# Performance work log

Measured on AMD Instinct MI355X. Metric: run time of the kernel, lower is better.

The kernel has to match this reference:

```python
import jax, jax.numpy as jnp
import numpy as np

D_MODEL = 1024
D_INNER = 2048   # expand=2
D_STATE = 16
D_CONV = 4
DT_RANK = 64     # ceil(d_model/16)
B_SZ = 2
L_SEQ = 2048
EPS = 1e-6


def setup_inputs() -> dict:
    key = jax.random.key(0)
    ks = jax.random.split(key, 9)
    def g(k, shape, scale=0.02):
        return jax.random.normal(k, shape, jnp.float32) * scale
    return {
        "x": jax.random.normal(ks[0], (B_SZ, L_SEQ, D_MODEL), jnp.float32),
        "ln_gamma": jnp.ones((D_MODEL,), jnp.float32),
        "ln_beta": jnp.zeros((D_MODEL,), jnp.float32),
        "in_proj_w": g(ks[1], (2 * D_INNER, D_MODEL)),
        "conv_w": g(ks[2], (D_INNER, 1, D_CONV), 0.1),
        "conv_b": g(ks[3], (D_INNER,), 0.1),
        "x_proj_w": g(ks[4], (DT_RANK + 2 * D_STATE, D_INNER)),
        "dt_proj_w": g(ks[5], (D_INNER, DT_RANK), 0.1),
        "dt_proj_b": g(ks[6], (D_INNER,), 0.1),
        "A_log": jnp.log(jnp.broadcast_to(jnp.arange(1, D_STATE + 1, dtype=jnp.float32), (D_INNER, D_STATE))),
        "D": jnp.ones((D_INNER,), jnp.float32),
        "out_proj_w": g(ks[7], (D_MODEL, D_INNER)),
    }


def _silu(v):
    return v * jax.nn.sigmoid(v)


def reference(x, ln_gamma, ln_beta, in_proj_w, conv_w, conv_b, x_proj_w,
              dt_proj_w, dt_proj_b, A_log, D, out_proj_w):
    B, L, _ = x.shape
    # LayerNorm (eps=1e-6)
    mu = x.mean(-1, keepdims=True)
    var = x.var(-1, keepdims=True)
    h = (x - mu) / jnp.sqrt(var + EPS) * ln_gamma + ln_beta
    # in_proj -> (B, 2*d_inner, L)
    xz = jnp.einsum('bld,ed->bel', h, in_proj_w)
    u, z = jnp.split(xz, 2, axis=1)
    # depthwise causal conv1d (padding=d_conv-1, then [..., :L]) + SiLU
    up = jnp.pad(u, ((0, 0), (0, 0), (D_CONV - 1, 0)))
    uc = jax.lax.conv_general_dilated(
        up, conv_w, (1,), 'VALID',
        dimension_numbers=('NCH', 'OIH', 'NCH'),
        feature_group_count=D_INNER)
    uc = _silu(uc + conv_b[None, :, None])  # (B, d_inner, L)
    # x_proj -> dt, B, C
    x_dbl = jnp.einsum('bdl,ed->ble', uc, x_proj_w)
    dt, Bm, Cm = jnp.split(x_dbl, [DT_RANK, DT_RANK + D_STATE], axis=-1)
    delta = jnp.einsum('blr,dr->bdl', dt, dt_proj_w) + dt_proj_b[None, :, None]
    delta = jax.nn.softplus(delta)  # delta_softplus=True with dt_proj bias
    A = -jnp.exp(A_log)  # (d_inner, d_state)
    deltaA = jnp.exp(jnp.einsum('bdl,dn->bdln', delta, A))
    Bm = jnp.transpose(Bm, (0, 2, 1))  # (B, n, L)
    Cm = jnp.transpose(Cm, (0, 2, 1))  # (B, n, L)
    deltaB_u = jnp.einsum('bdl,bnl,bdl->bdln', delta, Bm, uc)

    def step(state, inp):
        dA, dBu, Ct = inp  # (B,d,n), (B,d,n), (B,n)
        state = dA * state + dBu
        y = jnp.einsum('bdn,bn->bd', state, Ct)
        return state, y

    init = jnp.zeros((B, D_INNER, D_STATE), jnp.float32)
    _, ys = jax.lax.scan(
        step, init,
        (jnp.moveaxis(deltaA, 2, 0), jnp.moveaxis(deltaB_u, 2, 0), jnp.moveaxis(Cm, 2, 0)))
    y = jnp.moveaxis(ys, 0, 2)  # (B, d_inner, L)
    y = y + uc * D[None, :, None]
    y = y * _silu(z)
    out = jnp.einsum('bdl,ed->ble', y, out_proj_w)
    return out + x  # residual
```

## Files before the change

### kernel.cpp

```cpp
#include <hip/hip_runtime.h>
#include <hip/hip_bf16.h>

#define D_MODEL 1024
#define D_INNER 2048
#define D_STATE 16
#define D_CONV  4
#define DT_RANK 64
#define B_SZ    2
#define L_SEQ   2048
#define NTOK    (B_SZ * L_SEQ)
#define XD      (DT_RANK + 2 * D_STATE)
#define NCHUNK  64
#define TC      (L_SEQ / NCHUNK)
#define SPLITK  8

#define WS_U     0
#define WS_Z     16777216
#define WS_UC    33554432
#define WS_DY    50331648
#define WS_XDBL  67108864
#define WS_FLAG  67895296
#define WS_NEED  67895552
#define WS_W     67895552
#define OFF_INW  0
#define OFF_OUTW 8388608
#define OFF_XW   12582912
#define OFF_DTW  12976128
#define WS_FULL  81133824

typedef __attribute__((ext_vector_type(8))) short short8;
typedef __attribute__((ext_vector_type(4))) float float4v;

#define GAS __attribute__((address_space(1)))
#define LAS __attribute__((address_space(3)))
__device__ __forceinline__ void gload_lds16(const ushort* g, ushort* l) {
    __builtin_amdgcn_global_load_lds((const GAS uint*)g, (LAS uint*)l, 16, 0, 0);
}

__device__ __forceinline__ float bf2f_u(ushort u) {
    union { uint i; float f; } c; c.i = ((uint)u) << 16; return c.f;
}
__device__ __forceinline__ float u2f(uint u) {
    union { uint i; float f; } c; c.i = u; return c.f;
}
__device__ __forceinline__ ushort f2bf_u(float f) {
    union { float f; uint i; } c; c.f = f;
    uint r = c.i + 0x7FFFu + ((c.i >> 16) & 1u);
    return (ushort)(r >> 16);
}
__device__ __forceinline__ float silu_f(float v) {
    return v * __builtin_amdgcn_rcpf(1.f + __expf(-v));
}
__device__ __forceinline__ float softplus_f(float v) {
    return (v > 15.f) ? v : __logf(1.f + __expf(v));
}
__device__ __forceinline__ int sniff_bf16(const ushort* __restrict__ x) {
    int cnt = 0;
    #pragma unroll
    for (int i = 0; i < 128; i += 2) {
        int e = (x[i] >> 7) & 0xFF;
        cnt += (e >= 120 && e <= 129) ? 1 : 0;
    }
    return cnt >= 32 ? 1 : 0;
}
__device__ __forceinline__ float ldf(const void* p, size_t i, int isbf) {
    return isbf ? bf2f_u(((const ushort*)p)[i]) : ((const float*)p)[i];
}
__device__ __forceinline__ void unpack8(uint4 q, float* v) {
    v[0] = u2f(q.x << 16); v[1] = u2f(q.x & 0xFFFF0000u);
    v[2] = u2f(q.y << 16); v[3] = u2f(q.y & 0xFFFF0000u);
    v[4] = u2f(q.z << 16); v[5] = u2f(q.z & 0xFFFF0000u);
    v[6] = u2f(q.w << 16); v[7] = u2f(q.w & 0xFFFF0000u);
}

__global__ __launch_bounds__(64) void flag_kernel(const ushort* __restrict__ x, int* flag) {
    if (threadIdx.x == 0) *flag = sniff_bf16(x);
}
__global__ __launch_bounds__(256) void ws_marker_kernel(ushort* out, int n, float enc) {
    int i = blockIdx.x * 256 + threadIdx.x;
    if (i < n) out[i] = (i == 0) ? f2bf_u(enc) : (ushort)0;
}
__global__ __launch_bounds__(256) void cvt_kernel(
    const float* __restrict__ src, ushort* __restrict__ dst, int n8)
{
    int i = blockIdx.x * 256 + threadIdx.x;
    if (i >= n8) return;
    const float* s = src + (size_t)i * 8;
    float4 f0 = *(const float4*)s, f1 = *(const float4*)(s + 4);
    ushort o[8];
    o[0] = f2bf_u(f0.x); o[1] = f2bf_u(f0.y); o[2] = f2bf_u(f0.z); o[3] = f2bf_u(f0.w);
    o[4] = f2bf_u(f1.x); o[5] = f2bf_u(f1.y); o[6] = f2bf_u(f1.z); o[7] = f2bf_u(f1.w);
    *(uint4*)(dst + (size_t)i * 8) = *(const uint4*)o;
}

__global__ __launch_bounds__(256) void ln_kernel(
    const void* __restrict__ x, const void* __restrict__ gamma,
    const void* __restrict__ beta, ushort* __restrict__ h,
    const int* __restrict__ wsflag)
{
    int isbf = *wsflag;
    int t = blockIdx.x;
    int tid = threadIdx.x;
    float v[4], s1 = 0.f, s2 = 0.f;
    if (isbf) {
        uint2 raw = *(const uint2*)((const ushort*)x + (size_t)t * D_MODEL + tid * 4);
        const ushort* rs = (const ushort*)&raw;
        #pragma unroll
        for (int i = 0; i < 4; i++) v[i] = bf2f_u(rs[i]);
    } else {
        float4 raw = *(const float4*)((const float*)x + (size_t)t * D_MODEL + tid * 4);
        v[0] = raw.x; v[1] = raw.y; v[2] = raw.z; v[3] = raw.w;
    }
    #pragma unroll
    for (int i = 0; i < 4; i++) { s1 += v[i]; s2 += v[i] * v[i]; }
    #pragma unroll
    for (int off = 32; off; off >>= 1) { s1 += __shfl_down(s1, off); s2 += __shfl_down(s2, off); }
    __shared__ float red1[4], red2[4];
    __shared__ float stats[2];
    int wid = tid >> 6, lane = tid & 63;
    if (lane == 0) { red1[wid] = s1; red2[wid] = s2; }
    __syncthreads();
    if (tid == 0) {
        float a = 0.f, b = 0.f;
        #pragma unroll
        for (int i = 0; i < 4; i++) { a += red1[i]; b += red2[i]; }
        float mu = a * (1.f / D_MODEL);
        float var = b * (1.f / D_MODEL) - mu * mu;
        stats[0] = mu; stats[1] = rsqrtf(var + 1e-6f);
    }
    __syncthreads();
    float mu = stats[0], rstd = stats[1];
    ushort ov[4];
    #pragma unroll
    for (int i = 0; i < 4; i++) {
        float g = ldf(gamma, tid * 4 + i, isbf), bt = ldf(beta, tid * 4 + i, isbf);
        ov[i] = f2bf_u((v[i] - mu) * rstd * g + bt);
    }
    *(uint2*)(h + (size_t)t * D_MODEL + tid * 4) = *(const uint2*)ov;
}

template<int MODE>
__global__ __launch_bounds__(256) void gemm_nt(
    const ushort* __restrict__ A, int lda,
    const void* __restrict__ Bw, const void* __restrict__ Bc, int ldb,
    void* __restrict__ C, int ldc,
    int N, int K,
    const void* __restrict__ bias,
    const void* __restrict__ resid,
    void* __restrict__ C2,
    const int* __restrict__ wsflag)
{
    int isbf = *wsflag;
    const ushort* Bu = (Bc != nullptr && !isbf) ? (const ushort*)Bc : (const ushort*)Bw;
    int bfw = (Bc != nullptr) || isbf;
    __shared__ __align__(16) ushort LB[16384];

    int bx = blockIdx.x, by = blockIdx.y;
    if (MODE == 4) {
        int bid = by * 32 + bx;
        int xcd = bid & 7, w = bid >> 3;
        int pn = w & 7, pm = w >> 3;
        by = (xcd >> 2) * 16 + pm;
        bx = (xcd & 3) * 8 + pn;
    }
    if (MODE == 3) {
        int bid = by * 8 + bx;
        int xcd = bid & 7, w = bid >> 3;
        by = xcd * 4 + (w & 3);
        bx = w >> 2;
    }
    int m0 = by * 128, n0 = bx * 128;
    int kz = (MODE == 5) ? blockIdx.z : 0;
    int kbase = (MODE == 5) ? kz * 256 : 0;

    int tid = threadIdx.x;
    int lane = tid & 63, wid = tid >> 6;
    int wm = wid & 1, wn = wid >> 1;
    int lm = lane & 15, quad = lane >> 4;

    int S0 = wid * 64 + lane;
    int S1 = S0 + 256;
    int r0 = S0 >> 2, r1 = S1 >> 2;
    int cp0 = (S0 & 3) ^ ((S0 >> 3) & 3);
    int cp1 = (S1 & 3) ^ ((S1 >> 3) & 3);
    int ldsOffA0 = (wid * 64) * 8;
    int ldsOffA1 = (256 + wid * 64) * 8;

    const ushort* ga0 = A + (size_t)(m0 + r0) * lda + kbase + cp0 * 8;
    const ushort* ga1 = A + (size_t)(m0 + r1) * lda + kbase + cp1 * 8;
    int nr0 = n0 + r0; if (nr0 > N - 1) nr0 = N - 1;
    int nr1 = n0 + r1; if (nr1 > N - 1) nr1 = N - 1;
    const ushort* gb0 = Bu + (size_t)nr0 * ldb + kbase + cp0 * 8;
    const ushort* gb1 = Bu + (size_t)nr1 * ldb + kbase + cp1 * 8;

    int nk = K >> 5;

    auto issue = [&](int ki) {
        ushort* buf = LB + (ki & 1) * 8192;
        int ko = ki * 32;
        gload_lds16(ga0 + ko, buf + ldsOffA0);
        gload_lds16(ga1 + ko, buf + ldsOffA1);
        if (bfw) {
            gload_lds16(gb0 + ko, buf + 4096 + ldsOffA0);
            gload_lds16(gb1 + ko, buf + 4096 + ldsOffA1);
        } else {
            for (int q = tid; q < 512; q += 256) {
                int S = q, r = S >> 2;
                int cp = (S & 3) ^ ((S >> 3) & 3);
                int nr = n0 + r; if (nr > N - 1) nr = N - 1;
                const float* bp = (const float*)Bw + (size_t)nr * ldb + kbase + ko + cp * 8;
                float4 f0 = *(const float4*)bp, f1 = *(const float4*)(bp + 4);
                ushort tb[8];
                tb[0] = f2bf_u(f0.x); tb[1] = f2bf_u(f0.y); tb[2] = f2bf_u(f0.z); tb[3] = f2bf_u(f0.w);
                tb[4] = f2bf_u(f1.x); tb[5] = f2bf_u(f1.y); tb[6] = f2bf_u(f1.z); tb[7] = f2bf_u(f1.w);
                *(uint4*)(buf + 4096 + (size_t)S * 8) = *(const uint4*)tb;
            }
        }
    };

    float4v acc[4][4];
    #pragma unroll
    for (int i = 0; i < 4; i++)
        #pragma unroll
        for (int j = 0; j < 4; j++)
            acc[i][j] = (float4v){0.f, 0.f, 0.f, 0.f};

    issue(0);
    for (int ki = 0; ki < nk; ki++) {
        __syncthreads();
        if (ki + 1 < nk) issue(ki + 1);
        const ushort* As = LB + (ki & 1) * 8192;
        const ushort* Bs = As + 4096;
        short8 af[4], bfr[4];
        #pragma unroll
        for (int i = 0; i < 4; i++) {
            int r = wm * 64 + i * 16 + lm;
            int cpp = quad ^ ((r >> 1) & 3);
            af[i] = *(const short8*)(As + ((size_t)r * 4 + cpp) * 8);
        }
        #pragma unroll
        for (int j = 0; j < 4; j++) {
            int r = wn * 64 + j * 16 + lm;
            int cpp = quad ^ ((r >> 1) & 3);
            bfr[j] = *(const short8*)(Bs + ((size_t)r * 4 + cpp) * 8);
        }
        #pragma unroll
        for (int i = 0; i < 4; i++)
            #pragma unroll
            for (int j = 0; j < 4; j++)
                acc[i][j] = __builtin_amdgcn_mfma_f32_16x16x32_bf16(af[i], bfr[j], acc[i][j], 0, 0, 0);
    }
    __syncthreads();

    if (MODE == 5) {
        float* Ctf = (float*)LB;
        #pragma unroll
        for (int pass = 0; pass < 2; pass++) {
            if (wm == pass) {
                #pragma unroll
                for (int i = 0; i < 4; i++)
                    #pragma unroll
                    for (int j = 0; j < 4; j++) {
                        int col = wn * 64 + j * 16 + lm;
                        if (col < XD) {
                            #pragma unroll
                            for (int r = 0; r < 4; r++)
                                Ctf[(i * 16 + quad * 4 + r) * 100 + col] = acc[i][j][r];
                        }
                    }
            }
            __syncthreads();
            #pragma unroll
            for (int s = 0; s < 6; s++) {
                int idx = tid + 256 * s;
                int row = idx / 24, q4 = idx - row * 24;
                float4 v = *(const float4*)(Ctf + row * 100 + q4 * 4);
                *(float4*)((float*)C + ((size_t)kz * NTOK + m0 + pass * 64 + row) * XD + q4 * 4) = v;
            }
            __syncthreads();
        }
        return;
    }

    #pragma unroll
    for (int pass = 0; pass < 2; pass++) {
        if (wm == pass) {
            #pragma unroll
            for (int i = 0; i < 4; i++)
                #pragma unroll
                for (int j = 0; j < 4; j++) {
                    int col = wn * 64 + j * 16 + lm;
                    #pragma unroll
                    for (int r = 0; r < 4; r++) {
                        float v = acc[i][j][r];
                        if (MODE == 2) {
                            v += ldf(bias, n0 + col, isbf);
                            v = softplus_f(v);
                        }
                        LB[(size_t)(i * 16 + quad * 4 + r) * 136 + col] = f2bf_u(v);
                    }
                }
        }
        __syncthreads();
        int rb = m0 + pass * 64;
        if (MODE == 3) {
            if (isbf) {
                #pragma unroll
                for (int s = 0; s < 4; s++) {
                    int idx = tid + 256 * s;
                    int row = idx >> 4, q4 = idx & 15;
                    uint4 cv = *(const uint4*)(LB + (size_t)row * 136 + q4 * 8);
                    uint4 rv = *(const uint4*)((const ushort*)resid + (size_t)(rb + row) * ldc + n0 + q4 * 8);
                    float cf[8], rf[8];
                    unpack8(cv, cf); unpack8(rv, rf);
                    ushort o[8];
                    #pragma unroll
                    for (int e = 0; e < 8; e++) o[e] = f2bf_u(cf[e] + rf[e]);
                    *(uint4*)((ushort*)C + (size_t)(rb + row) * ldc + n0 + q4 * 8) = *(const uint4*)o;
                }
            } else {
                #pragma unroll
                for (int s = 0; s < 8; s++) {
                    int idx = tid + 256 * s;
                    int row = idx >> 5, q4 = idx & 31;
                    uint2 cv = *(const uint2*)(LB + (size_t)row * 136 + q4 * 4);
                    float4 rv = *(const float4*)((const float*)resid + (size_t)(rb + row) * ldc + n0 + q4 * 4);
                    float4 o;
                    o.x = u2f(cv.x << 16)          + rv.x;
                    o.y = u2f(cv.x & 0xFFFF0000u)  + rv.y;
                    o.z = u2f(cv.y << 16)          + rv.z;
                    o.w = u2f(cv.y & 0xFFFF0000u)  + rv.w;
                    *(float4*)((float*)C + (size_t)(rb + row) * ldc + n0 + q4 * 4) = o;
                }
            }
        } else {
            ushort* dst; int colb, ldd;
            if (MODE == 4) {
                dst = (n0 < D_INNER) ? (ushort*)C : (ushort*)C2;
                colb = n0 & (D_INNER - 1); ldd = D_INNER;
            } else {
                dst = (ushort*)C; colb = n0; ldd = ldc;
            }
            #pragma unroll
            for (int s = 0; s < 4; s++) {
                int idx = tid + 256 * s;
                int row = idx >> 4, q4 = idx & 15;
                uint4 cv = *(const uint4*)(LB + (size_t)row * 136 + q4 * 8);
                *(uint4*)(dst + (size_t)(rb + row) * ldd + colb + q4 * 8) = cv;
            }
        }
        __syncthreads();
    }
}

__global__ __launch_bounds__(256) void xproj_reduce(
    const float* __restrict__ part, ushort* __restrict__ xdbl)
{
    int i = blockIdx.x * 256 + threadIdx.x;
    float s = 0.f;
    #pragma unroll
    for (int kz = 0; kz < SPLITK; kz++)
        s += part[(size_t)kz * (NTOK * XD) + i];
    xdbl[i] = f2bf_u(s);
}

__global__ __launch_bounds__(256) void conv_silu_kernel(
    const ushort* __restrict__ u, const void* __restrict__ cw,
    const void* __restrict__ cb, ushort* __restrict__ uc,
    const int* __restrict__ wsflag)
{
    int isbf = *wsflag;
    int gid = blockIdx.x * 256 + threadIdx.x;
    int t = gid >> 11, d = gid & 2047;
    int l = t & (L_SEQ - 1);
    float acc = ldf(cb, d, isbf);
    #pragma unroll
    for (int k = 0; k < 4; k++) {
        int lp = l - 3 + k;
        if (lp >= 0)
            acc += bf2f_u(u[(size_t)(t - 3 + k) * 2048 + d]) * ldf(cw, d * 4 + k, isbf);
    }
    uc[gid] = f2bf_u(silu_f(acc));
}

__global__ __launch_bounds__(256) void scan_phase1(
    const ushort* __restrict__ delta, const ushort* __restrict__ uc,
    const ushort* __restrict__ xdbl,
    ushort* __restrict__ aprod, ushort* __restrict__ spart)
{
    int b = blockIdx.z, c = blockIdx.y;
    int d = blockIdx.x * 256 + threadIdx.x;
    float st[16];
    #pragma unroll
    for (int n = 0; n < 16; n++) st[n] = 0.f;
    float P = 1.f;
    int t0 = b * L_SEQ + c * TC;
    for (int i = 0; i < TC; ++i) {
        int t = t0 + i;
        float dlt = bf2f_u(delta[(size_t)t * 2048 + d]);
        float uv  = bf2f_u(uc[(size_t)t * 2048 + d]);
        float Bv[16];
        unpack8(*(const uint4*)(xdbl + (size_t)t * XD + DT_RANK), Bv);
        unpack8(*(const uint4*)(xdbl + (size_t)t * XD + DT_RANK + 8), Bv + 8);
        float du = dlt * uv;
        float E = __expf(-dlt);
        P *= E;
        float E2 = E * E, E4 = E2 * E2, E8 = E4 * E4;
        float c1 = E, c2 = E2, c3 = E * E2, c4 = E4;
        float c5 = E4 * E, c6 = E4 * E2, c7 = E4 * c3, c8 = E8;
        float c9 = E8 * E, c10 = E8 * E2, c11 = E8 * c3, c12 = E8 * E4;
        float c13 = E8 * c5, c14 = E8 * c6, c15 = E8 * c7, c16 = E8 * E8;
        st[0]  = c1  * st[0]  + du * Bv[0];
        st[1]  = c2  * st[1]  + du * Bv[1];
        st[2]  = c3  * st[2]  + du * Bv[2];
        st[3]  = c4  * st[3]  + du * Bv[3];
        st[4]  = c5  * st[4]  + du * Bv[4];
        st[5]  = c6  * st[5]  + du * Bv[5];
        st[6]  = c7  * st[6]  + du * Bv[6];
        st[7]  = c8  * st[7]  + du * Bv[7];
        st[8]  = c9  * st[8]  + du * Bv[8];
        st[9]  = c10 * st[9]  + du * Bv[9];
        st[10] = c11 * st[10] + du * Bv[10];
        st[11] = c12 * st[11] + du * Bv[11];
        st[12] = c13 * st[12] + du * Bv[12];
        st[13] = c14 * st[13] + du * Bv[13];
        st[14] = c15 * st[14] + du * Bv[14];
        st[15] = c16 * st[15] + du * Bv[15];
    }
    size_t base = ((size_t)((b * NCHUNK + c) * D_INNER + d)) * 16;
    ushort apb[16], stb[16];
    {
        float P2 = P * P, P4 = P2 * P2, P8 = P4 * P4;
        float q1 = P, q2 = P2, q3 = P * P2, q4 = P4;
        float q5 = P4 * P, q6 = P4 * P2, q7 = P4 * q3, q8 = P8;
        float q9 = P8 * P, q10 = P8 * P2, q11 = P8 * q3, q12 = P8 * P4;
        float q13 = P8 * q5, q14 = P8 * q6, q15 = P8 * q7, q16 = P8 * P8;
        apb[0] = f2bf_u(q1);  apb[1] = f2bf_u(q2);  apb[2] = f2bf_u(q3);  apb[3] = f2bf_u(q4);
        apb[4] = f2bf_u(q5);  apb[5] = f2bf_u(q6);  apb[6] = f2bf_u(q7);  apb[7] = f2bf_u(q8);
        apb[8] = f2bf_u(q9);  apb[9] = f2bf_u(q10); apb[10] = f2bf_u(q11); apb[11] = f2bf_u(q12);
        apb[12] = f2bf_u(q13); apb[13] = f2bf_u(q14); apb[14] = f2bf_u(q15); apb[15] = f2bf_u(q16);
    }
    #pragma unroll
    for (int n = 0; n < 16; n++) stb[n] = f2bf_u(st[n]);
    *(uint4*)(aprod + base)     = *(const uint4*)apb;
    *(uint4*)(aprod + base + 8) = *(const uint4*)(apb + 8);
    *(uint4*)(spart + base)     = *(const uint4*)stb;
    *(uint4*)(spart + base + 8) = *(const uint4*)(stb + 8);
}

__global__ __launch_bounds__(256) void scan_phase2(
    const ushort* __restrict__ aprod, ushort* __restrict__ spart)
{
    size_t i = (size_t)blockIdx.x * 256 + threadIdx.x;
    int b = (int)(i >> 15);
    size_t r = i & 32767;
    float s = 0.f;
    for (int c = 0; c < NCHUNK; ++c) {
        size_t idx = ((size_t)(b * NCHUNK + c) << 15) + r;
        float init = s;
        s = bf2f_u(aprod[idx]) * s + bf2f_u(spart[idx]);
        spart[idx] = f2bf_u(init);
    }
}

__global__ __launch_bounds__(256) void scan_phase3(
    ushort* dy, const ushort* __restrict__ uc,
    const ushort* __restrict__ xdbl, const ushort* __restrict__ z,
    const void* __restrict__ Dp, const ushort* __restrict__ spart,
    const int* __restrict__ wsflag)
{
    int isbf = *wsflag;
    int b = blockIdx.z, c = blockIdx.y;
    int d = blockIdx.x * 256 + threadIdx.x;
    float st[16];
    size_t base = ((size_t)((b * NCHUNK + c) * D_INNER + d)) * 16;
    unpack8(*(const uint4*)(spart + base), st);
    unpack8(*(const uint4*)(spart + base + 8), st + 8);
    float Dv = ldf(Dp, d, isbf);
    int t0 = b * L_SEQ + c * TC;
    for (int i = 0; i < TC; ++i) {
        int t = t0 + i;
        float dlt = bf2f_u(dy[(size_t)t * 2048 + d]);
        float uv  = bf2f_u(uc[(size_t)t * 2048 + d]);
        float Bv[16], Cv[16];
        unpack8(*(const uint4*)(xdbl + (size_t)t * XD + DT_RANK), Bv);
        unpack8(*(const uint4*)(xdbl + (size_t)t * XD + DT_RANK + 8), Bv + 8);
        unpack8(*(const uint4*)(xdbl + (size_t)t * XD + DT_RANK + 16), Cv);
        unpack8(*(const uint4*)(xdbl + (size_t)t * XD + DT_RANK + 24), Cv + 8);
        float du = dlt * uv;
        float E = __expf(-dlt);
        float E2 = E * E, E4 = E2 * E2, E8 = E4 * E4;
        float c1 = E, c2 = E2, c3 = E * E2, c4 = E4;
        float c5 = E4 * E, c6 = E4 * E2, c7 = E4 * c3, c8 = E8;
        float c9 = E8 * E, c10 = E8 * E2, c11 = E8 * c3, c12 = E8 * E4;
        float c13 = E8 * c5, c14 = E8 * c6, c15 = E8 * c7, c16 = E8 * E8;
        float p = 0.f;
        st[0]  = c1  * st[0]  + du * Bv[0];  p += st[0]  * Cv[0];
        st[1]  = c2  * st[1]  + du * Bv[1];  p += st[1]  * Cv[1];
        st[2]  = c3  * st[2]  + du * Bv[2];  p += st[2]  * Cv[2];
        st[3]  = c4  * st[3]  + du * Bv[3];  p += st[3]  * Cv[3];
        st[4]  = c5  * st[4]  + du * Bv[4];  p += st[4]  * Cv[4];
        st[5]  = c6  * st[5]  + du * Bv[5];  p += st[5]  * Cv[5];
        st[6]  = c7  * st[6]  + du * Bv[6];  p += st[6]  * Cv[6];
        st[7]  = c8  * st[7]  + du * Bv[7];  p += st[7]  * Cv[7];
        st[8]  = c9  * st[8]  + du * Bv[8];  p += st[8]  * Cv[8];
        st[9]  = c10 * st[9]  + du * Bv[9];  p += st[9]  * Cv[9];
        st[10] = c11 * st[10] + du * Bv[10]; p += st[10] * Cv[10];
        st[11] = c12 * st[11] + du * Bv[11]; p += st[11] * Cv[11];
        st[12] = c13 * st[12] + du * Bv[12]; p += st[12] * Cv[12];
        st[13] = c14 * st[13] + du * Bv[13]; p += st[13] * Cv[13];
        st[14] = c15 * st[14] + du * Bv[14]; p += st[14] * Cv[14];
        st[15] = c16 * st[15] + du * Bv[15]; p += st[15] * Cv[15];
        float zv = bf2f_u(z[(size_t)t * 2048 + d]);
        dy[(size_t)t * 2048 + d] = f2bf_u((p + uv * Dv) * silu_f(zv));
    }
}

extern "C" void kernel_launch(void* const* d_in, const int* in_sizes, int n_in,
                              void* d_out, int out_size, void* d_ws, size_t ws_size,
                              hipStream_t stream) {
    const void* x         = d_in[0];
    const void* ln_gamma  = d_in[1];
    const void* ln_beta   = d_in[2];
    const void* in_proj_w = d_in[3];
    const void* conv_w    = d_in[4];
    const void* conv_b    = d_in[5];
    const void* x_proj_w  = d_in[6];
    const void* dt_proj_w = d_in[7];
    const void* dt_proj_b = d_in[8];
    const void* Dp        = d_in[10];
    const void* out_proj_w= d_in[11];
    const ushort* xraw    = (const ushort*)d_in[0];

    if (ws_size < (size_t)WS_NEED) {
        float enc = 1000.f + (float)(ws_size >> 20);
        ws_marker_kernel<<<(out_size + 255) / 256, 256, 0, stream>>>((ushort*)d_out, out_size, enc);
        return;
    }
    const bool haveW = ws_size >= (size_t)WS_FULL;

    char* ws = (char*)d_ws;
    ushort* u      = (ushort*)(ws + WS_U);
    ushort* z      = (ushort*)(ws + WS_Z);
    ushort* uc     = (ushort*)(ws + WS_UC);
    ushort* dy     = (ushort*)(ws + WS_DY);
    ushort* xdbl   = (ushort*)(ws + WS_XDBL);
    int*    wsflag = (int*)(ws + WS_FLAG);
    float*  xpart  = (float*)(ws + WS_U);
    ushort* aprod  = (ushort*)(ws + WS_U);
    ushort* spart  = (ushort*)(ws + WS_U + 8388608);
    ushort* w_in   = haveW ? (ushort*)(ws + WS_W + OFF_INW)  : nullptr;
    ushort* w_out  = haveW ? (ushort*)(ws + WS_W + OFF_OUTW) : nullptr;
    ushort* w_x    = haveW ? (ushort*)(ws + WS_W + OFF_XW)   : nullptr;
    ushort* w_dt   = haveW ? (ushort*)(ws + WS_W + OFF_DTW)  : nullptr;

    flag_kernel<<<1, 64, 0, stream>>>(xraw, wsflag);

    if (haveW) {
        cvt_kernel<<<(4194304/8 + 255)/256, 256, 0, stream>>>((const float*)in_proj_w,  w_in,  4194304/8);
        cvt_kernel<<<(2097152/8 + 255)/256, 256, 0, stream>>>((const float*)out_proj_w, w_out, 2097152/8);
        cvt_kernel<<<( 196608/8 + 255)/256, 256, 0, stream>>>((const float*)x_proj_w,   w_x,    196608/8);
        cvt_kernel<<<( 131072/8 + 255)/256, 256, 0, stream>>>((const float*)dt_proj_w,  w_dt,   131072/8);
    }

    ln_kernel<<<NTOK, 256, 0, stream>>>(x, ln_gamma, ln_beta, dy, wsflag);

    gemm_nt<4><<<dim3(32, 32), 256, 0, stream>>>(
        dy, D_MODEL, in_proj_w, w_in, D_MODEL, u, D_INNER,
        2 * D_INNER, D_MODEL, nullptr, nullptr, z, wsflag);

    conv_silu_kernel<<<(NTOK * D_INNER) / 256, 256, 0, stream>>>(u, conv_w, conv_b, uc, wsflag);

    gemm_nt<5><<<dim3(1, 32, SPLITK), 256, 0, stream>>>(
        uc, D_INNER, x_proj_w, w_x, D_INNER, xpart, XD,
        XD, D_INNER / SPLITK, nullptr, nullptr, nullptr, wsflag);
    xproj_reduce<<<(NTOK * XD) / 256, 256, 0, stream>>>(xpart, xdbl);

    gemm_nt<2><<<dim3(16, 32), 256, 0, stream>>>(
        xdbl, XD, dt_proj_w, w_dt, DT_RANK, dy, D_INNER,
        D_INNER, DT_RANK, dt_proj_b, nullptr, nullptr, wsflag);

    scan_phase1<<<dim3(D_INNER / 256, NCHUNK, B_SZ), 256, 0, stream>>>(
        dy, uc, xdbl, aprod, spart);
    scan_phase2<<<(B_SZ * D_INNER * D_STATE) / 256, 256, 0, stream>>>(aprod, spart);
    scan_phase3<<<dim3(D_INNER / 256, NCHUNK, B_SZ), 256, 0, stream>>>(
        dy, uc, xdbl, z, Dp, spart, wsflag);

    gemm_nt<3><<<dim3(8, 32), 256, 0, stream>>>(
        dy, D_INNER, out_proj_w, w_out, D_INNER, d_out, D_MODEL,
        D_MODEL, D_INNER, nullptr, x, nullptr, wsflag);
}
```

Measured before the change: 341.7 us.

## Add 256x256-tile triple-buffered MFMA GEMM for in_proj with XCD-aware block mapping

Replaces the generic in_proj GEMM with a dedicated 512-thread kernel using 256x256 output tiles. It triple-buffers K-slices in LDS through direct global-to-LDS loads, uses XOR-swizzled LDS layouts, and remaps blocks across XCDs for L2 locality. The epilogue stages bf16 results through LDS for coalesced stores. The aim is more operand reuse per load and better overlap of loads with MFMA work, in exchange for higher register and LDS use and a path that only runs when converted weights exist.

```diff
diff --git a/kernel.cpp b/kernel.cpp
--- a/kernel.cpp
+++ b/kernel.cpp
@@ -137,6 +137,130 @@
         ov[i] = f2bf_u((v[i] - mu) * rstd * g + bt);
     }
     *(uint2*)(h + (size_t)t * D_MODEL + tid * 4) = *(const uint2*)ov;
+}
+
+#define TILE_STEP(BC, BS)                                                    \
+    do {                                                                     \
+        const ushort* ba = &LB[BC][0][0];                                    \
+        const ushort* bb = &LB[BC][1][0];                                    \
+        short8 av[8]; short8 bv[4];                                          \
+        _Pragma("unroll")                                                    \
+        for (int mf = 0; mf < 8; mf++)                                       \
+            av[mf] = *(const short8*)(ba + offA + mf * 512);                 \
+        _Pragma("unroll")                                                    \
+        for (int nf = 0; nf < 4; nf++)                                       \
+            bv[nf] = *(const short8*)(bb + offB + nf * 512);                 \
+        {                                                                    \
+            int ko = ((kt + 2) & 31) * 32;                                   \
+            ushort* sa = &LB[BS][0][wid * 1024];                             \
+            ushort* sb = &LB[BS][1][wid * 1024];                             \
+            gload_lds16(gA + ko, sa);                                        \
+            gload_lds16(gA + ko + 16 * 1024, sa + 512);                      \
+            gload_lds16(gB + ko, sb);                                        \
+            gload_lds16(gB + ko + 16 * 1024, sb + 512);                      \
+        }                                                                    \
+        __builtin_amdgcn_s_setprio(1);                                       \
+        _Pragma("unroll")                                                    \
+        for (int mf = 0; mf < 8; mf++)                                       \
+            _Pragma("unroll")                                                \
+            for (int nf = 0; nf < 4; nf++)                                   \
+                acc[mf][nf] = __builtin_amdgcn_mfma_f32_16x16x32_bf16(       \
+                    av[mf], bv[nf], acc[mf][nf], 0, 0, 0);                   \
+        __builtin_amdgcn_s_setprio(0);                                       \
+        asm volatile("s_waitcnt vmcnt(4)");                                  \
+        __builtin_amdgcn_s_barrier();                                        \
+        __builtin_amdgcn_sched_barrier(0);                                   \
+        kt++;                                                                \
+    } while (0)
+
+__global__ __launch_bounds__(512, 2) void gemm256_inproj(
+    const ushort* __restrict__ A,
+    const ushort* __restrict__ Bw,
+    ushort* __restrict__ U, ushort* __restrict__ Z)
+{
+    __shared__ __align__(16) ushort LB[3][2][8192];
+
+    int bid = blockIdx.y * 16 + blockIdx.x;
+    int xcd = bid & 7, w = bid >> 3;
+    int by = (xcd >> 1) * 4 + (w >> 3);
+    int bx = (xcd & 1) * 8 + (w & 7);
+    int m0 = by * 256, n0 = bx * 256;
+
+    int tid = threadIdx.x;
+    int lane = tid & 63, wid = tid >> 6;
+    int wm = wid & 1, wn = wid >> 1;
+    int lm = lane & 15, quad = lane >> 4;
+
+    int sr = lane >> 2;
+    int srow = wid * 32 + sr;
+    int sc = ((lane & 3) ^ ((srow >> 1) & 3)) << 3;
+    const ushort* gA = A + (size_t)(m0 + srow) * 1024 + sc;
+    const ushort* gB = Bw + (size_t)(n0 + srow) * 1024 + sc;
+
+    int posq = (quad ^ ((lm >> 1) & 3)) << 3;
+    int offA = (wm * 128 + lm) * 32 + posq;
+    int offB = (wn * 64 + lm) * 32 + posq;
+
+    float4v acc[8][4];
+    #pragma unroll
+    for (int i = 0; i < 8; i++)
+        #pragma unroll
+        for (int j = 0; j < 4; j++)
+            acc[i][j] = (float4v){0.f, 0.f, 0.f, 0.f};
+
+    {
+        ushort* sa = &LB[0][0][wid * 1024];
+        ushort* sb = &LB[0][1][wid * 1024];
+        gload_lds16(gA, sa);
+        gload_lds16(gA + 16 * 1024, sa + 512);
+        gload_lds16(gB, sb);
+        gload_lds16(gB + 16 * 1024, sb + 512);
+        sa = &LB[1][0][wid * 1024];
+        sb = &LB[1][1][wid * 1024];
+        gload_lds16(gA + 32, sa);
+        gload_lds16(gA + 32 + 16 * 1024, sa + 512);
+        gload_lds16(gB + 32, sb);
+        gload_lds16(gB + 32 + 16 * 1024, sb + 512);
+    }
+    asm volatile("s_waitcnt vmcnt(4)");
+    __builtin_amdgcn_s_barrier();
+    __builtin_amdgcn_sched_barrier(0);
+
+    int kt = 0;
+    #pragma unroll 1
+    for (int it = 0; it < 10; it++) {
+        TILE_STEP(0, 2);
+        TILE_STEP(1, 0);
+        TILE_STEP(2, 1);
+    }
+    TILE_STEP(0, 2);
+    TILE_STEP(1, 0);
+
+    __syncthreads();
+    ushort* eb = &LB[0][0][0];
+    ushort* dst = (n0 < D_INNER) ? U : Z;
+    int cn = n0 & (D_INNER - 1);
+    int rl = lane >> 3, cl = (lane & 7) * 8;
+    #pragma unroll
+    for (int pass = 0; pass < 2; pass++) {
+        if (pass) __syncthreads();
+        if (wm == pass) {
+            ushort* ep = eb + wn * (128 * 72);
+            #pragma unroll
+            for (int mf = 0; mf < 8; mf++)
+                #pragma unroll
+                for (int nf = 0; nf < 4; nf++)
+                    #pragma unroll
+                    for (int r = 0; r < 4; r++)
+                        ep[(mf * 16 + quad * 4 + r) * 72 + nf * 16 + lm] = f2bf_u(acc[mf][nf][r]);
+            #pragma unroll
+            for (int itr = 0; itr < 16; itr++) {
+                int row = itr * 8 + rl;
+                uint4 v = *(const uint4*)(ep + row * 72 + cl);
+                *(uint4*)(dst + (size_t)(m0 + pass * 128 + row) * D_INNER + cn + wn * 64 + cl) = v;
+            }
+        }
+    }
 }
 
 template<int MODE>
@@ -565,9 +689,13 @@
 
     ln_kernel<<<NTOK, 256, 0, stream>>>(x, ln_gamma, ln_beta, dy, wsflag);
 
-    gemm_nt<4><<<dim3(32, 32), 256, 0, stream>>>(
-        dy, D_MODEL, in_proj_w, w_in, D_MODEL, u, D_INNER,
-        2 * D_INNER, D_MODEL, nullptr, nullptr, z, wsflag);
+    if (haveW) {
+        gemm256_inproj<<<dim3(16, 16), 512, 0, stream>>>(dy, w_in, u, z);
+    } else {
+        gemm_nt<4><<<dim3(32, 32), 256, 0, stream>>>(
+            dy, D_MODEL, in_proj_w, w_in, D_MODEL, u, D_INNER,
+            2 * D_INNER, D_MODEL, nullptr, nullptr, z, wsflag);
+    }
 
     conv_silu_kernel<<<(NTOK * D_INNER) / 256, 256, 0, stream>>>(u, conv_w, conv_b, uc, wsflag);
 
```

Result: slower. 374.0 us (+9.5%).
